# Optimization experiments

Hardware: AMD Instinct MI355X
Metric: run time of the kernel (lower is better)

## Reference

```python
import jax, jax.numpy as jnp
import numpy as np

ALPHA, GAMMA, EPS, BIG = 0.25, 2.0, 1e-7, 1e7
STRIDES = (8, 16, 32, 64, 128)
SHRINK = 0.2


def _project(boxes, fw, fh, stride):
    # shrink box around its center by SHRINK, project to feature grid (floor/ceil), clip
    cx = (boxes[..., 0] + boxes[..., 2]) * 0.5
    cy = (boxes[..., 1] + boxes[..., 3]) * 0.5
    hw = (boxes[..., 2] - boxes[..., 0]) * 0.5 * SHRINK
    hh = (boxes[..., 3] - boxes[..., 1]) * 0.5 * SHRINK
    x1 = jnp.clip(jnp.floor((cx - hw) / stride).astype(jnp.int32), 0, fw - 1)
    y1 = jnp.clip(jnp.floor((cy - hh) / stride).astype(jnp.int32), 0, fh - 1)
    x2 = jnp.clip(jnp.ceil((cx + hw) / stride).astype(jnp.int32), 1, fw)
    y2 = jnp.clip(jnp.ceil((cy + hh) / stride).astype(jnp.int32), 1, fh)
    return x1, y1, x2, y2


def _level_loss(cls_l, regr_l, boxes, labels, stride, fh, fw):
    # cls_l [B,fh,fw,C], regr_l [B,fh,fw,4], boxes [B,G,4], labels [B,G] -> loss [B,G]
    B, G = labels.shape
    x1, y1, x2, y2 = _project(boxes, fw, fh, stride)
    xs = jnp.arange(fw, dtype=jnp.int32)
    ys = jnp.arange(fh, dtype=jnp.int32)
    mx = (xs[None, None] >= x1[..., None]) & (xs[None, None] < x2[..., None])  # [B,G,fw]
    my = (ys[None, None] >= y1[..., None]) & (ys[None, None] < y2[..., None])  # [B,G,fh]
    mask = my[..., :, None] & mx[..., None, :]                                 # [B,G,fh,fw]
    denom = jnp.maximum(jnp.sum(mask, axis=(2, 3)).astype(cls_l.dtype), 1.0)   # = #positives

    # focal over one-hot(gt_label): sum_c = f0 - neg[gt] + pos[gt]
    p = jnp.clip(cls_l, EPS, 1.0 - EPS)
    neg = (1.0 - ALPHA) * p ** GAMMA * (-jnp.log1p(-p))   # per-class label=0 term
    pos = ALPHA * (1.0 - p) ** GAMMA * (-jnp.log(p))      # per-class label=1 term
    f0 = jnp.sum(neg, axis=-1)                            # [B,fh,fw]
    bidx = jnp.arange(B)[:, None]
    neg_g = neg[bidx, :, :, labels]                       # [B,G,fh,fw]
    pos_g = pos[bidx, :, :, labels]                       # [B,G,fh,fw]
    focal_map = f0[:, None] - neg_g + pos_g
    loss_cls = jnp.sum(jnp.where(mask, focal_map, 0.0), axis=(2, 3)) / denom

    # iou loss on (l,t,r,b)/(4*stride) targets, mean over region
    sx = (xs.astype(cls_l.dtype) + 0.5) * stride          # [fw]
    sy = (ys.astype(cls_l.dtype) + 0.5) * stride          # [fh]
    s = 1.0 / (4.0 * stride)
    tl = jnp.maximum(sx[None, None, None] - boxes[..., 0, None, None], 0.0) * s    # [B,G,1,fw]
    tt = jnp.maximum(sy[None, None, :, None] - boxes[..., 1, None, None], 0.0) * s  # [B,G,fh,1]
    tr = jnp.maximum(boxes[..., 2, None, None] - sx[None, None, None], 0.0) * s     # [B,G,1,fw]
    tb = jnp.maximum(boxes[..., 3, None, None] - sy[None, None, :, None], 0.0) * s  # [B,G,fh,1]
    pl = regr_l[..., 0][:, None]   # [B,1,fh,fw]
    pt = regr_l[..., 1][:, None]
    pr = regr_l[..., 2][:, None]
    pb = regr_l[..., 3][:, None]
    t_area = (tl + tr) * (tt + tb)                        # [B,G,fh,fw]
    p_area = (pl + pr) * (pt + pb)                        # [B,1,fh,fw]
    w_i = jnp.minimum(pl, tl) + jnp.minimum(pr, tr)
    h_i = jnp.minimum(pb, tb) + jnp.minimum(pt, tt)
    a_i = w_i * h_i
    a_u = t_area + p_area - a_i
    iou_map = -jnp.log((a_i + EPS) / (a_u + EPS))
    loss_iou = jnp.sum(jnp.where(mask, iou_map, 0.0), axis=(2, 3)) / denom

    empty = (x1 == x2) | (y1 == y2)                       # tf.cond 'do_not_match' branch
    return jnp.where(empty, BIG, loss_cls + loss_iou)


def _all_level_losses(cls_pred, regr_pred, gt_boxes, feature_shapes):
    fs = np.asarray(feature_shapes)
    B, C = cls_pred.shape[0], cls_pred.shape[-1]
    labels = jnp.clip(gt_boxes[..., 4].astype(jnp.int32), 0, C - 1)
    boxes = gt_boxes[..., :4]
    losses, start = [], 0
    for i, stride in enumerate(STRIDES):
        fh, fw = int(fs[i, 0]), int(fs[i, 1])
        cls_l = cls_pred[:, start:start + fh * fw].reshape(B, fh, fw, C)
        regr_l = regr_pred[:, start:start + fh * fw].reshape(B, fh, fw, 4)
        losses.append(_level_loss(cls_l, regr_l, boxes, labels, float(stride), fh, fw))
        start += fh * fw
    return jnp.stack(losses, axis=-1)   # [B,G,L]


def setup_inputs():
    key = jax.random.key(0)
    k = jax.random.split(key, 7)
    B, G, C = 8, 64, 80
    feature_shapes = np.array([[128, 128], [64, 64], [32, 32], [16, 16], [8, 8]], dtype=np.int32)
    total = int(np.prod(feature_shapes, axis=-1).sum())   # 21824 locations (1024x1024 img)
    cls_pred = jax.random.uniform(k[0], (B, total, C), jnp.float32, 0.01, 0.99)
    regr_pred = jax.random.uniform(k[1], (B, total, 4), jnp.float32, 0.05, 2.0)
    cx = jax.random.uniform(k[2], (B, G), jnp.float32, 64.0, 960.0)
    cy = jax.random.uniform(k[3], (B, G), jnp.float32, 64.0, 960.0)
    w = jax.random.uniform(k[4], (B, G), jnp.float32, 32.0, 320.0)
    h = jax.random.uniform(k[5], (B, G), jnp.float32, 32.0, 320.0)
    x1 = jnp.clip(cx - w / 2, 0.0, 1024.0)
    y1 = jnp.clip(cy - h / 2, 0.0, 1024.0)
    x2 = jnp.clip(cx + w / 2, 0.0, 1024.0)
    y2 = jnp.clip(cy + h / 2, 0.0, 1024.0)
    lbl = jax.random.randint(k[6], (B, G), 0, C).astype(jnp.float32)
    gt_boxes = jnp.stack([x1, y1, x2, y2, lbl], axis=-1)
    keep = (jnp.arange(G) < G - 16).astype(jnp.float32)   # last 16 rows are zero padding
    gt_boxes = gt_boxes * keep[None, :, None]
    return {"cls_pred": cls_pred, "regr_pred": regr_pred,
            "feature_shapes": feature_shapes, "gt_boxes": gt_boxes}


def reference(cls_pred, regr_pred, feature_shapes, gt_boxes):
    losses = _all_level_losses(cls_pred, regr_pred, gt_boxes, feature_shapes)   # [B,G,L]
    levels = jnp.argmin(losses, axis=-1).astype(jnp.int32)                      # [B,G]
    valid = jnp.sum(jnp.abs(gt_boxes[..., :4]), axis=-1) > 0                    # trim_padding_boxes
    levels = jnp.where(valid, levels, -1)                                       # padded boxes -> -1
    return levels.reshape(-1)
```

## Files before the change

kernel.cpp:

```cpp
#include <hip/hip_runtime.h>
#include <math.h>

static constexpr int B = 8;
static constexpr int G = 64;
static constexpr int C = 80;
static constexpr int TOTAL = 21824;
static constexpr float EPSF = 1e-7f;
static constexpr float BIGF = 1e7f;

__device__ __forceinline__ double wave_sum_d(double v) {
#pragma unroll
    for (int off = 32; off > 0; off >>= 1)
        v += __shfl_xor(v, off, 64);
    return v;
}

__device__ __forceinline__ float neg_fast(float x) {
    float p = fminf(fmaxf(x, EPSF), 1.0f - EPSF);
    float nl = -__logf(1.0f - p);
    return 0.75f * p * p * nl;
}

__global__ __launch_bounds__(256) void f0_kernel(const float* __restrict__ cls,
                                                 float* __restrict__ f0) {
    int idx = (int)(blockIdx.x * blockDim.x + threadIdx.x);
    if (idx >= B * TOTAL) return;
    const float4* p = (const float4*)(cls + (size_t)idx * C);
    double acc = 0.0;
#pragma unroll 4
    for (int i = 0; i < C / 4; ++i) {
        float4 v = p[i];
        acc += (double)neg_fast(v.x);
        acc += (double)neg_fast(v.y);
        acc += (double)neg_fast(v.z);
        acc += (double)neg_fast(v.w);
    }
    f0[idx] = (float)acc;
}

__global__ __launch_bounds__(256) void level_loss_kernel(
        const float* __restrict__ cls, const float* __restrict__ regr,
        const float* __restrict__ gt, const float* __restrict__ f0,
        float* __restrict__ losses) {
    const int   fws[5]     = {128, 64, 32, 16, 8};
    const int   offs[5]    = {0, 16384, 20480, 21504, 21760};
    const float strides[5] = {8.f, 16.f, 32.f, 64.f, 128.f};

    int wave = (int)((blockIdx.x * blockDim.x + threadIdx.x) >> 6);
    int lane = (int)(threadIdx.x & 63);
    if (wave >= B * G * 5) return;
    int boxid = wave / 5;
    int l     = wave - boxid * 5;

    const float* box = gt + (size_t)boxid * 5;
    float b0 = box[0], b1 = box[1], b2 = box[2], b3 = box[3];
    if (fabsf(b0) + fabsf(b1) + fabsf(b2) + fabsf(b3) <= 0.0f) return;

    int label = (int)box[4];
    label = min(max(label, 0), C - 1);
    int b = boxid / G;

    float cx = (b0 + b2) * 0.5f, cy = (b1 + b3) * 0.5f;
    float hw = (b2 - b0) * 0.5f * 0.2f, hh = (b3 - b1) * 0.5f * 0.2f;

    const float st = strides[l];
    const int fw = fws[l];
    int x1 = min(max((int)floorf((cx - hw) / st), 0), fw - 1);
    int y1 = min(max((int)floorf((cy - hh) / st), 0), fw - 1);
    int x2 = min(max((int)ceilf((cx + hw) / st), 1), fw);
    int y2 = min(max((int)ceilf((cy + hh) / st), 1), fw);

    float loss;
    if (x1 == x2 || y1 == y2) {
        loss = BIGF;
    } else {
        int rw = x2 - x1;
        int area = rw * (y2 - y1);
        double sf = 0.0, si = 0.0;
        float s = 1.0f / (4.0f * st);
        for (int idx = lane; idx < area; idx += 64) {
            int yy = y1 + idx / rw;
            int xx = x1 + idx % rw;
            int loc = offs[l] + yy * fw + xx;
            size_t base = (size_t)b * TOTAL + (size_t)loc;
            float pv = cls[base * C + label];
            float p = fminf(fmaxf(pv, EPSF), 1.0f - EPSF);
            float neg_g = 0.75f * p * p * (-log1pf(-p));
            float omp = 1.0f - p;
            float pos_g = 0.25f * omp * omp * (-logf(p));
            sf += (double)((f0[base] - neg_g) + pos_g);
            const float4 r = *(const float4*)(regr + base * 4);
            float sx = ((float)xx + 0.5f) * st;
            float sy = ((float)yy + 0.5f) * st;
            float tl = fmaxf(sx - b0, 0.0f) * s;
            float tt = fmaxf(sy - b1, 0.0f) * s;
            float tr = fmaxf(b2 - sx, 0.0f) * s;
            float tb = fmaxf(b3 - sy, 0.0f) * s;
            float t_area = (tl + tr) * (tt + tb);
            float p_area = (r.x + r.z) * (r.y + r.w);
            float w_i = fminf(r.x, tl) + fminf(r.z, tr);
            float h_i = fminf(r.w, tb) + fminf(r.y, tt);
            float a_i = w_i * h_i;
            float a_u = (t_area + p_area) - a_i;
            si += (double)(-logf((a_i + EPSF) / (a_u + EPSF)));
        }
        sf = wave_sum_d(sf);
        si = wave_sum_d(si);
        float denom = (float)area;
        loss = (float)sf / denom + (float)si / denom;
    }
    if (lane == 0) losses[boxid * 5 + l] = loss;
}

__global__ __launch_bounds__(256) void argmin_kernel(
        const float* __restrict__ gt, const float* __restrict__ losses,
        int* __restrict__ out) {
    int boxid = (int)(blockIdx.x * blockDim.x + threadIdx.x);
    if (boxid >= B * G) return;
    const float* box = gt + (size_t)boxid * 5;
    if (fabsf(box[0]) + fabsf(box[1]) + fabsf(box[2]) + fabsf(box[3]) <= 0.0f) {
        out[boxid] = -1;
        return;
    }
    float best = losses[boxid * 5];
    int bestl = 0;
#pragma unroll
    for (int l = 1; l < 5; ++l) {
        float v = losses[boxid * 5 + l];
        if (v < best) { best = v; bestl = l; }
    }
    out[boxid] = bestl;
}

extern "C" void kernel_launch(void* const* d_in, const int* in_sizes, int n_in,
                              void* d_out, int out_size, void* d_ws, size_t ws_size,
                              hipStream_t stream) {
    const float* cls  = (const float*)d_in[0];
    const float* regr = (const float*)d_in[1];
    const float* gt   = (const float*)d_in[3];

    float* f0     = (float*)d_ws;
    float* losses = (float*)((char*)d_ws + 702464);

    int nloc = B * TOTAL;
    f0_kernel<<<dim3((nloc + 255) / 256), dim3(256), 0, stream>>>(cls, f0);

    int nwaves = B * G * 5;
    level_loss_kernel<<<dim3((nwaves * 64) / 256), dim3(256), 0, stream>>>(
        cls, regr, gt, f0, losses);

    argmin_kernel<<<dim3(2), dim3(256), 0, stream>>>(gt, losses, (int*)d_out);
}
```

Baseline: 104.5 us.

## Stage cls rows through LDS for coalesced f0 loads and fuse argmin into loss

After: 102.6 us. About the same (-1.9%).

```diff
diff --git a/kernel.cpp b/kernel.cpp
--- a/kernel.cpp
+++ b/kernel.cpp
@@ -7,6 +7,9 @@
 static constexpr int TOTAL = 21824;
 static constexpr float EPSF = 1e-7f;
 static constexpr float BIGF = 1e7f;
+
+static constexpr int LOCS = 128;
+static constexpr int PAD  = 84;
 
 __device__ __forceinline__ double wave_sum_d(double v) {
 #pragma unroll
@@ -21,41 +24,54 @@
     return 0.75f * p * p * nl;
 }
 
-__global__ __launch_bounds__(256) void f0_kernel(const float* __restrict__ cls,
+__global__ __launch_bounds__(128) void f0_kernel(const float* __restrict__ cls,
                                                  float* __restrict__ f0) {
-    int idx = (int)(blockIdx.x * blockDim.x + threadIdx.x);
-    if (idx >= B * TOTAL) return;
-    const float4* p = (const float4*)(cls + (size_t)idx * C);
+    __shared__ float lds[LOCS * PAD];
+    const int t = (int)threadIdx.x;
+    const size_t baseLoc = (size_t)blockIdx.x * LOCS;
+    const float4* gsrc = (const float4*)(cls + baseLoc * C);
+
+#pragma unroll
+    for (int r = 0; r < 20; ++r) {
+        int q = r * LOCS + t;
+        float4 v = gsrc[q];
+        int loc = q / 20, chunk = q - loc * 20;
+        *(float4*)&lds[loc * PAD + chunk * 4] = v;
+    }
+    __syncthreads();
+
     double acc = 0.0;
-#pragma unroll 4
-    for (int i = 0; i < C / 4; ++i) {
-        float4 v = p[i];
+    const float* row = &lds[t * PAD];
+#pragma unroll
+    for (int i = 0; i < 20; ++i) {
+        float4 v = *(const float4*)&row[i * 4];
         acc += (double)neg_fast(v.x);
         acc += (double)neg_fast(v.y);
         acc += (double)neg_fast(v.z);
         acc += (double)neg_fast(v.w);
     }
-    f0[idx] = (float)acc;
+    f0[baseLoc + t] = (float)acc;
 }
 
-__global__ __launch_bounds__(256) void level_loss_kernel(
+__global__ __launch_bounds__(320) void select_kernel(
         const float* __restrict__ cls, const float* __restrict__ regr,
         const float* __restrict__ gt, const float* __restrict__ f0,
-        float* __restrict__ losses) {
+        int* __restrict__ out) {
     const int   fws[5]     = {128, 64, 32, 16, 8};
     const int   offs[5]    = {0, 16384, 20480, 21504, 21760};
     const float strides[5] = {8.f, 16.f, 32.f, 64.f, 128.f};
 
-    int wave = (int)((blockIdx.x * blockDim.x + threadIdx.x) >> 6);
-    int lane = (int)(threadIdx.x & 63);
-    if (wave >= B * G * 5) return;
-    int boxid = wave / 5;
-    int l     = wave - boxid * 5;
+    __shared__ float lloss[5];
+    const int boxid = (int)blockIdx.x;
+    const int l     = (int)(threadIdx.x >> 6);
+    const int lane  = (int)(threadIdx.x & 63);
 
     const float* box = gt + (size_t)boxid * 5;
     float b0 = box[0], b1 = box[1], b2 = box[2], b3 = box[3];
-    if (fabsf(b0) + fabsf(b1) + fabsf(b2) + fabsf(b3) <= 0.0f) return;
-
+    if (fabsf(b0) + fabsf(b1) + fabsf(b2) + fabsf(b3) <= 0.0f) {
+        if (threadIdx.x == 0) out[boxid] = -1;
+        return;
+    }
     int label = (int)box[4];
     label = min(max(label, 0), C - 1);
     int b = boxid / G;
@@ -109,27 +125,19 @@
         float denom = (float)area;
         loss = (float)sf / denom + (float)si / denom;
     }
-    if (lane == 0) losses[boxid * 5 + l] = loss;
-}
+    if (lane == 0) lloss[l] = loss;
+    __syncthreads();
 
-__global__ __launch_bounds__(256) void argmin_kernel(
-        const float* __restrict__ gt, const float* __restrict__ losses,
-        int* __restrict__ out) {
-    int boxid = (int)(blockIdx.x * blockDim.x + threadIdx.x);
-    if (boxid >= B * G) return;
-    const float* box = gt + (size_t)boxid * 5;
-    if (fabsf(box[0]) + fabsf(box[1]) + fabsf(box[2]) + fabsf(box[3]) <= 0.0f) {
-        out[boxid] = -1;
-        return;
+    if (threadIdx.x == 0) {
+        float best = lloss[0];
+        int bestl = 0;
+#pragma unroll
+        for (int k = 1; k < 5; ++k) {
+            float v = lloss[k];
+            if (v < best) { best = v; bestl = k; }
+        }
+        out[boxid] = bestl;
     }
-    float best = losses[boxid * 5];
-    int bestl = 0;
-#pragma unroll
-    for (int l = 1; l < 5; ++l) {
-        float v = losses[boxid * 5 + l];
-        if (v < best) { best = v; bestl = l; }
-    }
-    out[boxid] = bestl;
 }
 
 extern "C" void kernel_launch(void* const* d_in, const int* in_sizes, int n_in,
@@ -139,15 +147,10 @@
     const float* regr = (const float*)d_in[1];
     const float* gt   = (const float*)d_in[3];
 
-    float* f0     = (float*)d_ws;
-    float* losses = (float*)((char*)d_ws + 702464);
+    float* f0 = (float*)d_ws;
 
-    int nloc = B * TOTAL;
-    f0_kernel<<<dim3((nloc + 255) / 256), dim3(256), 0, stream>>>(cls, f0);
+    f0_kernel<<<dim3((B * TOTAL) / LOCS), dim3(LOCS), 0, stream>>>(cls, f0);
 
-    int nwaves = B * G * 5;
-    level_loss_kernel<<<dim3((nwaves * 64) / 256), dim3(256), 0, stream>>>(
-        cls, regr, gt, f0, losses);
-
-    argmin_kernel<<<dim3(2), dim3(256), 0, stream>>>(gt, losses, (int*)d_out);
+    select_kernel<<<dim3(B * G), dim3(320), 0, stream>>>(cls, regr, gt, f0,
+                                                         (int*)d_out);
 }
```
